# Kernel optimization log

Hardware: AMD Instinct MI355X
Metric: run time of the kernel (lower is better)

The kernel has to match this reference:

```python
import jax, jax.numpy as jnp
import numpy as np

N_BLOCK = 3
N_NODES = 20000
N_EDGES = 320000
N_GRAPHS = 200
F = 128          # n_hidden_feat = n_GCN_feat
FE = 3 * F       # concat [ni, nj, delta]
K1 = 36          # N_shbf * N_srbf
K2 = 26          # plane-wave feature dim (hard-coded in source)


def setup_inputs() -> dict:
    key = jax.random.key(0)
    ks = jax.random.split(key, 20)
    s = 0.05
    inp = {
        "nodes": jax.random.normal(ks[0], (N_NODES, F), jnp.float32),
        "edge_sources": jax.random.randint(ks[1], (N_EDGES,), 0, N_NODES),
        "edge_targets": jax.random.randint(ks[2], (N_EDGES,), 0, N_NODES),
        # keep distances away from 0 to avoid blowing up (nj-ni)/rij
        "edge_distance": jax.random.uniform(ks[3], (N_EDGES,), jnp.float32, 0.5, 1.5),
        "graph_indices": jax.random.randint(ks[4], (N_NODES,), 0, N_GRAPHS),
        "node_counts": jnp.ones((N_GRAPHS,), jnp.float32) * (N_NODES / N_GRAPHS),
        "combine_sets": jax.random.normal(ks[5], (N_EDGES, K1), jnp.float32),
        "plane_wave": jax.random.normal(ks[6], (N_EDGES, K2), jnp.float32),
        # parameters ([in, out] layout; torch Linear has bias=False here)
        "W_emb": jax.random.normal(ks[7], (F, F), jnp.float32) * s,
        "Wg": jax.random.normal(ks[8], (N_BLOCK, FE, F), jnp.float32) * s,
        "Wm": jax.random.normal(ks[9], (N_BLOCK, FE, F), jnp.float32) * s,
        "W1v": jax.random.normal(ks[10], (N_BLOCK, K1, F), jnp.float32) * s,
        "W2v": jax.random.normal(ks[11], (N_BLOCK, K2, F), jnp.float32) * s,
        "W2vg": jax.random.normal(ks[12], (N_BLOCK, K2, F), jnp.float32) * s,
        "Wp1": jax.random.normal(ks[13], (N_BLOCK, F, F), jnp.float32) * s,
        "Wp2": jax.random.normal(ks[14], (N_BLOCK, F, F), jnp.float32) * s,
        "Wpsi": jax.random.normal(ks[15], (N_BLOCK, F, F), jnp.float32) * s,
        "Wlr1": jax.random.normal(ks[16], (F, F // 2), jnp.float32) * s,
        "Wlr2": jax.random.normal(ks[17], (F // 2, F // 3), jnp.float32) * s,
        "Wlr3": jax.random.normal(ks[18], (F // 3, 1), jnp.float32) * s,
    }
    return inp


def reference(nodes, edge_sources, edge_targets, edge_distance, graph_indices,
              node_counts, combine_sets, plane_wave,
              W_emb, Wg, Wm, W1v, W2v, W2vg, Wp1, Wp2, Wpsi, Wlr1, Wlr2, Wlr3):
    G = node_counts.shape[0]
    # NodeEmbedding: Linear + Sigmoid
    x = jax.nn.sigmoid(nodes @ W_emb)
    pools = []
    for i in range(N_BLOCK):
        # GatedGraphConvolution: edge gather -> concat -> gated MLP -> scatter-add
        ni = x[edge_sources]                      # [E, F]
        nj = x[edge_targets]                      # [E, F]
        delta = (nj - ni) / edge_distance[:, None]
        fe = jnp.concatenate([ni, nj, delta], axis=1)   # [E, 3F]
        e_gate = jax.nn.sigmoid(fe @ Wg[i])
        e_mlp = jax.nn.elu(fe @ Wm[i])
        z1 = combine_sets @ W1v[i]                # note: linear1_vector_gate unused in source forward
        z2 = (plane_wave @ W2v[i]) * jax.nn.sigmoid(plane_wave @ W2vg[i])
        z = e_gate * e_mlp * (z1 + z2)            # [E, F]
        x = x.at[edge_sources].add(z)             # output = input.clone(); index_add_
        # Gated_pooling (division by node_counts is discarded in the source -> plain segment sum)
        zp = jax.nn.elu(x @ Wp1[i])
        pools.append(jax.ops.segment_sum(zp * (x @ Wp2[i]), graph_indices, num_segments=G))
        # MLP_psi2n
        x = jax.nn.elu(x @ Wpsi[i])
    out = pools[0] + pools[1] + pools[2]          # sum over blocks, [G, F]
    out = jax.nn.elu(out @ Wlr1)
    out = jax.nn.elu(out @ Wlr2)
    out = out @ Wlr3                              # [G, 1]
    return out.squeeze()
```

## Files before the change

### kernel.cpp

```cpp
#include <hip/hip_runtime.h>
#include <math.h>

#define NNODES 20000
#define NEDGES 320000
#define NGRAPHS 200
#define K1 36
#define K2 26

struct WPtrs { const float* w[6]; };

__device__ __forceinline__ float sigf(float v) { return 1.0f / (1.0f + expf(-v)); }
__device__ __forceinline__ float eluf(float v) { return v > 0.0f ? v : expm1f(v); }

__global__ __launch_bounds__(256) void gemm128_kernel(
    const float* __restrict__ A, WPtrs wp, float* __restrict__ out,
    int out_stride, int act)
{
    __shared__ float4 Wl[2048];
    __shared__ float4 Al[2048];

    const int half  = blockIdx.y & 1;
    const int chunk = blockIdx.y >> 1;
    const float4* W4 = (const float4*)(wp.w[chunk] + half * 64);

    for (int idx = threadIdx.x; idx < 2048; idx += 256) {
        int k = idx >> 4, fq = idx & 15;
        Wl[idx] = W4[k * 32 + fq];
    }
    const int m0 = blockIdx.x * 64;
    const float4* A4 = (const float4*)A;
    for (int idx = threadIdx.x; idx < 2048; idx += 256) {
        int r = idx >> 5, k4 = idx & 31;
        int row = m0 + r;
        Al[idx] = (row < NNODES) ? A4[(size_t)row * 32 + k4] : make_float4(0.f, 0.f, 0.f, 0.f);
    }
    __syncthreads();

    const int fg = threadIdx.x & 15;
    const int ng = threadIdx.x >> 4;

    float acc[4][4] = {};
    #pragma unroll 4
    for (int k4 = 0; k4 < 32; ++k4) {
        float4 a[4], w[4];
        #pragma unroll
        for (int j = 0; j < 4; ++j) a[j] = Al[(ng * 4 + j) * 32 + k4];
        #pragma unroll
        for (int q = 0; q < 4; ++q) w[q] = Wl[(k4 * 4 + q) * 16 + fg];
        #pragma unroll
        for (int j = 0; j < 4; ++j) {
            const float* ap = (const float*)&a[j];
            #pragma unroll
            for (int q = 0; q < 4; ++q) {
                const float* wq = (const float*)&w[q];
                #pragma unroll
                for (int jj = 0; jj < 4; ++jj)
                    acc[j][jj] = fmaf(ap[q], wq[jj], acc[j][jj]);
            }
        }
    }

    const int coff = chunk * 128 + half * 64 + fg * 4;
    #pragma unroll
    for (int j = 0; j < 4; ++j) {
        int row = m0 + ng * 4 + j;
        if (row < NNODES) {
            float4 v; float* vp = (float*)&v;
            #pragma unroll
            for (int jj = 0; jj < 4; ++jj) {
                float t = acc[j][jj];
                vp[jj] = act ? sigf(t) : t;
            }
            *(float4*)(out + (size_t)row * out_stride + coff) = v;
        }
    }
}

__global__ __launch_bounds__(256, 2) void edge_kernel(
    const float* __restrict__ P,
    const int* __restrict__ esrc, const int* __restrict__ etgt,
    const float* __restrict__ dist,
    const float* __restrict__ cs, const float* __restrict__ pw,
    const float* __restrict__ W1v, const float* __restrict__ W2v,
    const float* __restrict__ W2vg,
    float* __restrict__ x)
{
    const int f    = threadIdx.x & 127;
    const int esub = threadIdx.x >> 7;

    float w1[K1], w2[K2], w2g[K2];
    #pragma unroll
    for (int k = 0; k < K1; ++k) w1[k]  = W1v[k * 128 + f];
    #pragma unroll
    for (int k = 0; k < K2; ++k) w2[k]  = W2v[k * 128 + f];
    #pragma unroll
    for (int k = 0; k < K2; ++k) w2g[k] = W2vg[k * 128 + f];
    #pragma unroll
    for (int k = 0; k < K1; ++k) asm volatile("" : "+v"(w1[k]));
    #pragma unroll
    for (int k = 0; k < K2; ++k) asm volatile("" : "+v"(w2[k]));
    #pragma unroll
    for (int k = 0; k < K2; ++k) asm volatile("" : "+v"(w2g[k]));

    const int ebase = blockIdx.x * 64 + esub;

    int e  = __builtin_amdgcn_readfirstlane(ebase);
    int s  = esrc[e];
    int t  = etgt[e];
    float d = dist[e];

    for (int it = 0; it < 32; ++it) {
        const float* Ps = P + (size_t)s * 768;
        const float* Pt = P + (size_t)t * 768;
        float g0 = Ps[f];
        float g1 = Pt[128 + f];
        float g2t = Pt[256 + f];
        float g2s = Ps[256 + f];
        float m0 = Ps[384 + f];
        float m1 = Pt[512 + f];
        float m2t = Pt[640 + f];
        float m2s = Ps[640 + f];

        const float* csr = cs + (size_t)e * K1;
        const float* pwr = pw + (size_t)e * K2;
        float z1 = 0.f, za = 0.f, zb = 0.f;
        #pragma unroll
        for (int k = 0; k < K1; ++k) z1 = fmaf(csr[k], w1[k], z1);
        #pragma unroll
        for (int k = 0; k < K2; ++k) {
            float p = pwr[k];
            za = fmaf(p, w2[k],  za);
            zb = fmaf(p, w2g[k], zb);
        }

        const float invd = 1.0f / d;
        const int scur = s;

        if (it < 31) {
            int en = __builtin_amdgcn_readfirstlane(ebase + (it + 1) * 2);
            s = esrc[en];
            t = etgt[en];
            d = dist[en];
            e = en;
        }

        float g = g0 + g1 + (g2t - g2s) * invd;
        float m = m0 + m1 + (m2t - m2s) * invd;
        float z = sigf(g) * eluf(m) * (z1 + za * sigf(zb));
        atomicAdd(x + (size_t)scur * 128 + f, z);
    }
}

__global__ __launch_bounds__(256) void pool_psi_kernel(
    const float* __restrict__ T, const int* __restrict__ gidx,
    float* __restrict__ pools, float* __restrict__ xout)
{
    int idx = blockIdx.x * 256 + threadIdx.x;
    int n = idx >> 7, f = idx & 127;
    float h1 = eluf(T[(size_t)n * 384 + f]);
    float h2 = T[(size_t)n * 384 + 128 + f];
    atomicAdd(pools + (size_t)gidx[n] * 128 + f, h1 * h2);
    xout[(size_t)n * 128 + f] = eluf(T[(size_t)n * 384 + 256 + f]);
}

__global__ __launch_bounds__(64) void final_kernel(
    const float* __restrict__ pools,
    const float* __restrict__ Wlr1, const float* __restrict__ Wlr2,
    const float* __restrict__ Wlr3, float* __restrict__ out)
{
    __shared__ float h1[64];
    __shared__ float h2[42];
    const int g = blockIdx.x;
    const int f = threadIdx.x;

    float a = 0.f;
    #pragma unroll 8
    for (int k = 0; k < 128; ++k) a = fmaf(pools[(size_t)g * 128 + k], Wlr1[k * 64 + f], a);
    h1[f] = eluf(a);
    __syncthreads();
    if (f < 42) {
        float b = 0.f;
        #pragma unroll
        for (int k = 0; k < 64; ++k) b = fmaf(h1[k], Wlr2[k * 42 + f], b);
        h2[f] = eluf(b);
    }
    __syncthreads();
    if (f == 0) {
        float c = 0.f;
        #pragma unroll
        for (int k = 0; k < 42; ++k) c = fmaf(h2[k], Wlr3[k], c);
        out[g] = c;
    }
}

__global__ void zero_kernel(float* p, int n)
{
    int i = blockIdx.x * 256 + threadIdx.x;
    if (i < n) p[i] = 0.f;
}

extern "C" void kernel_launch(void* const* d_in, const int* in_sizes, int n_in,
                              void* d_out, int out_size, void* d_ws, size_t ws_size,
                              hipStream_t stream)
{
    const float* nodes = (const float*)d_in[0];
    const int*   esrc  = (const int*)d_in[1];
    const int*   etgt  = (const int*)d_in[2];
    const float* dist  = (const float*)d_in[3];
    const int*   gidx  = (const int*)d_in[4];
    const float* cs    = (const float*)d_in[6];
    const float* pw    = (const float*)d_in[7];
    const float* W_emb = (const float*)d_in[8];
    const float* Wg    = (const float*)d_in[9];
    const float* Wm    = (const float*)d_in[10];
    const float* W1v   = (const float*)d_in[11];
    const float* W2v   = (const float*)d_in[12];
    const float* W2vg  = (const float*)d_in[13];
    const float* Wp1   = (const float*)d_in[14];
    const float* Wp2   = (const float*)d_in[15];
    const float* Wpsi  = (const float*)d_in[16];
    const float* Wlr1  = (const float*)d_in[17];
    const float* Wlr2  = (const float*)d_in[18];
    const float* Wlr3  = (const float*)d_in[19];
    float* outp = (float*)d_out;

    float* xA    = (float*)d_ws;
    float* xB    = xA + (size_t)NNODES * 128;
    float* P     = xB + (size_t)NNODES * 128;
    float* pools = P + (size_t)NNODES * 768;

    zero_kernel<<<100, 256, 0, stream>>>(pools, NGRAPHS * 128);

    {
        WPtrs wp{}; wp.w[0] = W_emb;
        gemm128_kernel<<<dim3(313, 2), 256, 0, stream>>>(nodes, wp, xA, 128, 1);
    }

    float* xc = xA;
    float* xn = xB;
    for (int i = 0; i < 3; ++i) {
        WPtrs wp{};
        const float* Wgi = Wg + (size_t)i * 49152;
        const float* Wmi = Wm + (size_t)i * 49152;
        wp.w[0] = Wgi;          wp.w[1] = Wgi + 16384;  wp.w[2] = Wgi + 32768;
        wp.w[3] = Wmi;          wp.w[4] = Wmi + 16384;  wp.w[5] = Wmi + 32768;
        gemm128_kernel<<<dim3(313, 12), 256, 0, stream>>>(xc, wp, P, 768, 0);

        edge_kernel<<<5000, 256, 0, stream>>>(P, esrc, etgt, dist, cs, pw,
            W1v + (size_t)i * (K1 * 128),
            W2v + (size_t)i * (K2 * 128),
            W2vg + (size_t)i * (K2 * 128), xc);

        WPtrs wq{};
        wq.w[0] = Wp1 + (size_t)i * 16384;
        wq.w[1] = Wp2 + (size_t)i * 16384;
        wq.w[2] = Wpsi + (size_t)i * 16384;
        gemm128_kernel<<<dim3(313, 6), 256, 0, stream>>>(xc, wq, P, 384, 0);

        pool_psi_kernel<<<10000, 256, 0, stream>>>(P, gidx, pools, xn);

        float* tmp = xc; xc = xn; xn = tmp;
    }

    final_kernel<<<NGRAPHS, 64, 0, stream>>>(pools, Wlr1, Wlr2, Wlr3, outp);
}
```

Measured before the change: 1.253 ms.

## Batch four edges per iteration in edge kernel and use fast math intrinsics

The edge kernel now processes four consecutive edges per wave iteration, issuing all index, gather, combine_sets and plane_wave loads for the batch together, instead of one edge at a time with a single-edge prefetch. The aim is more memory-level parallelism to hide gather latency. Sigmoid, ELU and 1/d now use the hardware rcp and __expf intrinsics, which trades some accuracy for cheaper math. The edge-to-wave mapping changes to contiguous groups of four, and register pressure rises, which may lower occupancy under the existing launch bounds.

```diff
diff --git a/kernel.cpp b/kernel.cpp
--- a/kernel.cpp
+++ b/kernel.cpp
@@ -11,6 +11,9 @@
 
 __device__ __forceinline__ float sigf(float v) { return 1.0f / (1.0f + expf(-v)); }
 __device__ __forceinline__ float eluf(float v) { return v > 0.0f ? v : expm1f(v); }
+
+__device__ __forceinline__ float fsig(float v) { return __builtin_amdgcn_rcpf(1.0f + __expf(-v)); }
+__device__ __forceinline__ float felu(float v) { return v > 0.0f ? v : __expf(v) - 1.0f; }
 
 __global__ __launch_bounds__(256) void gemm128_kernel(
     const float* __restrict__ A, WPtrs wp, float* __restrict__ out,
@@ -102,52 +105,62 @@
     #pragma unroll
     for (int k = 0; k < K2; ++k) asm volatile("" : "+v"(w2g[k]));
 
-    const int ebase = blockIdx.x * 64 + esub;
-
-    int e  = __builtin_amdgcn_readfirstlane(ebase);
-    int s  = esrc[e];
-    int t  = etgt[e];
-    float d = dist[e];
-
-    for (int it = 0; it < 32; ++it) {
-        const float* Ps = P + (size_t)s * 768;
-        const float* Pt = P + (size_t)t * 768;
-        float g0 = Ps[f];
-        float g1 = Pt[128 + f];
-        float g2t = Pt[256 + f];
-        float g2s = Ps[256 + f];
-        float m0 = Ps[384 + f];
-        float m1 = Pt[512 + f];
-        float m2t = Pt[640 + f];
-        float m2s = Ps[640 + f];
-
-        const float* csr = cs + (size_t)e * K1;
-        const float* pwr = pw + (size_t)e * K2;
-        float z1 = 0.f, za = 0.f, zb = 0.f;
-        #pragma unroll
-        for (int k = 0; k < K1; ++k) z1 = fmaf(csr[k], w1[k], z1);
+    const int base = blockIdx.x * 64 + esub * 4;
+
+    for (int it = 0; it < 8; ++it) {
+        const int e0 = __builtin_amdgcn_readfirstlane(base + it * 8);
+
+        int s[4], t[4];
+        float dd[4];
+        #pragma unroll
+        for (int u = 0; u < 4; ++u) {
+            s[u]  = esrc[e0 + u];
+            t[u]  = etgt[e0 + u];
+            dd[u] = dist[e0 + u];
+        }
+
+        float g0[4], g1[4], g2t[4], g2s[4], m0[4], m1[4], m2t[4], m2s[4];
+        #pragma unroll
+        for (int u = 0; u < 4; ++u) {
+            const float* Ps = P + (size_t)s[u] * 768;
+            const float* Pt = P + (size_t)t[u] * 768;
+            g0[u]  = Ps[f];
+            g2s[u] = Ps[256 + f];
+            m0[u]  = Ps[384 + f];
+            m2s[u] = Ps[640 + f];
+            g1[u]  = Pt[128 + f];
+            g2t[u] = Pt[256 + f];
+            m1[u]  = Pt[512 + f];
+            m2t[u] = Pt[640 + f];
+        }
+
+        float z1[4] = {}, za[4] = {}, zb[4] = {};
+        #pragma unroll
+        for (int k = 0; k < K1; ++k) {
+            const float wv = w1[k];
+            #pragma unroll
+            for (int u = 0; u < 4; ++u)
+                z1[u] = fmaf(cs[(size_t)(e0 + u) * K1 + k], wv, z1[u]);
+        }
         #pragma unroll
         for (int k = 0; k < K2; ++k) {
-            float p = pwr[k];
-            za = fmaf(p, w2[k],  za);
-            zb = fmaf(p, w2g[k], zb);
-        }
-
-        const float invd = 1.0f / d;
-        const int scur = s;
-
-        if (it < 31) {
-            int en = __builtin_amdgcn_readfirstlane(ebase + (it + 1) * 2);
-            s = esrc[en];
-            t = etgt[en];
-            d = dist[en];
-            e = en;
-        }
-
-        float g = g0 + g1 + (g2t - g2s) * invd;
-        float m = m0 + m1 + (m2t - m2s) * invd;
-        float z = sigf(g) * eluf(m) * (z1 + za * sigf(zb));
-        atomicAdd(x + (size_t)scur * 128 + f, z);
+            const float wa = w2[k], wb = w2g[k];
+            #pragma unroll
+            for (int u = 0; u < 4; ++u) {
+                const float p = pw[(size_t)(e0 + u) * K2 + k];
+                za[u] = fmaf(p, wa, za[u]);
+                zb[u] = fmaf(p, wb, zb[u]);
+            }
+        }
+
+        #pragma unroll
+        for (int u = 0; u < 4; ++u) {
+            const float invd = __builtin_amdgcn_rcpf(dd[u]);
+            const float g = g0[u] + g1[u] + (g2t[u] - g2s[u]) * invd;
+            const float m = m0[u] + m1[u] + (m2t[u] - m2s[u]) * invd;
+            const float z = fsig(g) * felu(m) * (z1[u] + za[u] * fsig(zb[u]));
+            atomicAdd(x + (size_t)s[u] * 128 + f, z);
+        }
     }
 }
 
```

New measurement: 1.280 ms. 2.1% more time.
